# Kernel optimization log

Measured on AMD Instinct MI355X. Metric: run time of the kernel, lower is better.

Reference implementation:

```python
import jax, jax.numpy as jnp
import numpy as np

B, T, D, H = 16384, 48, 32, 64  # batch, num_lags, input_dim(num_features), hidden_size


def setup_inputs() -> dict:
    key = jax.random.key(0)
    ks = jax.random.split(key, 8)
    s = 1.0 / np.sqrt(H)  # torch-style uniform bound magnitude, approximated via scaled normal
    return {
        "x": jax.random.normal(ks[0], (B, T, D), dtype=jnp.float32),
        "h0": jax.random.normal(ks[1], (B, H), dtype=jnp.float32) * 0.01,
        "c0": jax.random.normal(ks[2], (B, H), dtype=jnp.float32) * 0.01,
        "W_att": jax.random.normal(ks[3], (1, 2 * H + T), dtype=jnp.float32) * 0.05,
        "b_att": jnp.zeros((1,), dtype=jnp.float32),
        "W_ih": jax.random.normal(ks[4], (4 * H, D), dtype=jnp.float32) * s,
        "W_hh": jax.random.normal(ks[5], (4 * H, H), dtype=jnp.float32) * s,
        "b_ih": jnp.zeros((4 * H,), dtype=jnp.float32),
        "b_hh": jnp.zeros((4 * H,), dtype=jnp.float32),
    }


def reference(x, h0, c0, W_att, b_att, W_ih, W_hh, b_ih, b_hh):
    # x: [B, T, D];  input-attention DA-RNN encoder with single-layer LSTM.
    Bn, Tn, Dn = x.shape
    Hn = h0.shape[-1]
    xT = jnp.transpose(x, (0, 2, 1))  # [B, D, T] full per-feature series, constant over t
    w_att = W_att[0]                   # [2H+T]

    def step(carry, xt):
        ht, ct = carry  # [B, H]
        hrep = jnp.broadcast_to(ht[:, None, :], (Bn, Dn, Hn))
        crep = jnp.broadcast_to(ct[:, None, :], (Bn, Dn, Hn))
        feat = jnp.concatenate([hrep, crep, xT], axis=2)  # [B, D, 2H+T]
        et = jnp.einsum('bdf,f->bd', feat, w_att) + b_att[0]  # [B, D]
        at = jax.nn.softmax(et, axis=1)                        # softmax over features
        wi = at * xt                                           # [B, D]
        gates = wi @ W_ih.T + b_ih + ht @ W_hh.T + b_hh        # [B, 4H]
        i_g, f_g, g_g, o_g = jnp.split(gates, 4, axis=1)
        i_g = jax.nn.sigmoid(i_g)
        f_g = jax.nn.sigmoid(f_g)
        g_g = jnp.tanh(g_g)
        o_g = jax.nn.sigmoid(o_g)
        ct2 = f_g * ct + i_g * g_g
        ht2 = o_g * jnp.tanh(ct2)
        return (ht2, ct2), (at, ht2)

    xs = jnp.transpose(x, (1, 0, 2))  # [T, B, D]
    _, (ats, hts) = jax.lax.scan(step, (h0, c0), xs)
    attention = jnp.transpose(ats, (1, 0, 2))       # [B, T, D]
    input_encoded = jnp.transpose(hts, (1, 0, 2))   # [B, T, H]
    return attention, input_encoded
```

## Files before the change

kernel.cpp:

```cpp
#include <hip/hip_runtime.h>

#define TT 48
#define DD 32
#define HH 64
#define BB 16384
#define LOG2E 1.4426950408889634f

typedef __bf16 bf16x8 __attribute__((ext_vector_type(8)));
typedef float f32x4 __attribute__((ext_vector_type(4)));

#define MFMA(a, b, c) __builtin_amdgcn_mfma_f32_16x16x32_bf16(a, b, c, 0, 0, 0)
#define BC(v) __builtin_bit_cast(bf16x8, v)

static __device__ __forceinline__ float exp2_f(float v) {
#if __has_builtin(__builtin_amdgcn_exp2f)
  return __builtin_amdgcn_exp2f(v);
#else
  return exp2f(v);
#endif
}
static __device__ __forceinline__ unsigned short bfu(float f) {
  __bf16 b = (__bf16)f;
  return __builtin_bit_cast(unsigned short, b);
}
static __device__ __forceinline__ float sigm2(float y) {
  return __builtin_amdgcn_rcpf(1.f + exp2_f(-y));
}
static __device__ __forceinline__ float tanh2(float y) {
  return fmaf(-2.f, __builtin_amdgcn_rcpf(1.f + exp2_f(y)), 1.f);
}


__global__ void prep_kernel(const float* __restrict__ W_ih, const float* __restrict__ W_hh,
                            const float* __restrict__ b_ih, const float* __restrict__ b_hh,
                            unsigned short* __restrict__ WhhL, unsigned short* __restrict__ WihL,
                            float* __restrict__ bsumL) {
  const int tid = threadIdx.x;
  const int l = tid & 63, qt = tid >> 6;
  const int rowl = l & 15, kq = (l >> 4) * 8;
  for (int mm = 0; mm < 4; ++mm) {
    const int m = qt * 4 + mm;
    const int g = m >> 2, hq = m & 3;
    const float s = (g == 2) ? 2.f * LOG2E : LOG2E;
    const int hidx = (hq >> 1) * 32 + (rowl >> 2) * 8 + (hq & 1) * 4 + (rowl & 3);
    const int orig = g * 64 + hidx;
    for (int c = 0; c < 2; ++c)
      for (int j = 0; j < 8; ++j)
        WhhL[(m * 2 + c) * 512 + l * 8 + j] = bfu(W_hh[orig * 64 + c * 32 + kq + j] * s);
    for (int j = 0; j < 8; ++j)
      WihL[m * 512 + l * 8 + j] = bfu(W_ih[orig * 32 + kq + j] * s);
    if ((l >> 4) == 0) bsumL[m * 16 + rowl] = (b_ih[orig] + b_hh[orig]) * s;
  }
}

__global__ __launch_bounds__(256) void attn_kernel(const float* __restrict__ x,
                                                   const float* __restrict__ W_att,
                                                   float* __restrict__ out0) {
  int tid = threadIdx.x;
  int b = blockIdx.x * 32 + (tid >> 3);
  int dq = (tid & 7) * 4;
  const float* xb = x + (size_t)b * (TT * DD);
  float px = 0.f, py = 0.f, pz = 0.f, pw = 0.f;
#pragma unroll 4
  for (int t = 0; t < TT; ++t) {
    float w = W_att[2 * HH + t];
    float4 xv = *(const float4*)(xb + t * DD + dq);
    px = fmaf(xv.x, w, px);
    py = fmaf(xv.y, w, py);
    pz = fmaf(xv.z, w, pz);
    pw = fmaf(xv.w, w, pw);
  }
  float m = fmaxf(fmaxf(px, py), fmaxf(pz, pw));
#pragma unroll
  for (int s = 1; s < 8; s <<= 1) m = fmaxf(m, __shfl_xor(m, s));
  float ex = __expf(px - m), ey = __expf(py - m), ez = __expf(pz - m), ew = __expf(pw - m);
  float sum = ex + ey + ez + ew;
#pragma unroll
  for (int s = 1; s < 8; s <<= 1) sum += __shfl_xor(sum, s);
  float inv = __builtin_amdgcn_rcpf(sum);
  float4 a;
  a.x = ex * inv; a.y = ey * inv; a.z = ez * inv; a.w = ew * inv;
  float* o = out0 + (size_t)b * (TT * DD) + dq;
#pragma unroll 4
  for (int t = 0; t < TT; ++t) *(float4*)(o + t * DD) = a;
}

__global__ __launch_bounds__(256, 1) void lstm_kernel(
    const float* __restrict__ x, const float* __restrict__ h0, const float* __restrict__ c0,
    const float* __restrict__ a_src, const unsigned short* __restrict__ WhhL,
    const unsigned short* __restrict__ WihL, const float* __restrict__ bsumL,
    float* __restrict__ out1) {
  const int tid = threadIdx.x;
  const int l = tid & 63;
  const int wid = tid >> 6;
  const int b = l & 15;
  const int qp = l >> 4;
  const int brow = blockIdx.x * 64 + wid * 16 + b;

  f32x4 whhHi[16][2], wihR[16], biasR[16];
#pragma unroll
  for (int m = 0; m < 16; ++m) {
#pragma unroll
    for (int c = 0; c < 2; ++c)
      whhHi[m][c] = *(const f32x4*)(WhhL + ((m * 2 + c) << 9) + l * 8);
    wihR[m] = *(const f32x4*)(WihL + (m << 9) + l * 8);
    biasR[m] = *(const f32x4*)(bsumL + m * 16 + qp * 4);
  }
#pragma unroll
  for (int m = 0; m < 16; ++m) {
#pragma unroll
    for (int c = 0; c < 2; ++c) asm volatile("" : "+v"(whhHi[m][c]));
    asm volatile("" : "+a"(wihR[m]));
    asm volatile("" : "+a"(biasR[m]));
  }

  float av[8];
  {
    const float* ap = a_src + (size_t)brow * (TT * DD) + qp * 8;
    float4 a0 = *(const float4*)ap, a1 = *(const float4*)(ap + 4);
    av[0] = a0.x; av[1] = a0.y; av[2] = a0.z; av[3] = a0.w;
    av[4] = a1.x; av[5] = a1.y; av[6] = a1.z; av[7] = a1.w;
  }

  f32x4 creg[4];
#pragma unroll
  for (int hq = 0; hq < 4; ++hq)
    creg[hq] = *(const f32x4*)(c0 + (size_t)brow * HH + (hq >> 1) * 32 + qp * 8 + (hq & 1) * 4);

  bf16x8 bh[2];
#pragma unroll
  for (int c = 0; c < 2; ++c) {
    const float* hp = h0 + (size_t)brow * HH + c * 32 + qp * 8;
    float4 v0 = *(const float4*)hp, v1 = *(const float4*)(hp + 4);
    float vv[8] = {v0.x, v0.y, v0.z, v0.w, v1.x, v1.y, v1.z, v1.w};
#pragma unroll
    for (int j = 0; j < 8; ++j) bh[c][j] = (__bf16)vv[j];
  }

  const float* xp = x + (size_t)brow * (TT * DD) + qp * 8;
  float* op = out1 + (size_t)brow * (TT * HH);
  float xv[8];
  {
    float4 x0 = *(const float4*)xp, x1 = *(const float4*)(xp + 4);
    xv[0] = x0.x; xv[1] = x0.y; xv[2] = x0.z; xv[3] = x0.w;
    xv[4] = x1.x; xv[5] = x1.y; xv[6] = x1.z; xv[7] = x1.w;
  }

#pragma unroll 1
  for (int t = 0; t < TT; ++t) {
    bf16x8 bxw;
#pragma unroll
    for (int j = 0; j < 8; ++j) bxw[j] = (__bf16)(xv[j] * av[j]);
    const int tn = (t + 1 < TT) ? (t + 1) : (TT - 1);
    float xn[8];
    {
      const float* xnp = xp + (size_t)tn * DD;
      float4 x0 = *(const float4*)xnp, x1 = *(const float4*)(xnp + 4);
      xn[0] = x0.x; xn[1] = x0.y; xn[2] = x0.z; xn[3] = x0.w;
      xn[4] = x1.x; xn[5] = x1.y; xn[6] = x1.z; xn[7] = x1.w;
    }

    bf16x8 nbh[2];
#pragma unroll
    for (int hq = 0; hq < 4; ++hq) {
      f32x4 acc[4];
#pragma unroll
      for (int g = 0; g < 4; ++g) {
        const int m = g * 4 + hq;
        f32x4 A = MFMA(BC(whhHi[m][0]), bh[0], biasR[m]);
        A = MFMA(BC(whhHi[m][1]), bh[1], A);
        A = MFMA(BC(wihR[m]), bxw, A);
        acc[g] = A;
      }
      float hr[4];
#pragma unroll
      for (int r = 0; r < 4; ++r) {
        float ig = sigm2(acc[0][r]);
        float fg = sigm2(acc[1][r]);
        float gt = tanh2(acc[2][r]);
        float og = sigm2(acc[3][r]);
        float cn = fg * creg[hq][r] + ig * gt;
        creg[hq][r] = cn;
        hr[r] = og * tanh2(2.f * LOG2E * cn);
      }
      float4 hv;
      hv.x = hr[0]; hv.y = hr[1]; hv.z = hr[2]; hv.w = hr[3];
      *(float4*)(op + (size_t)t * HH + (hq >> 1) * 32 + qp * 8 + (hq & 1) * 4) = hv;
#pragma unroll
      for (int r = 0; r < 4; ++r) nbh[hq >> 1][(hq & 1) * 4 + r] = (__bf16)hr[r];
    }
    bh[0] = nbh[0];
    bh[1] = nbh[1];
#pragma unroll
    for (int j = 0; j < 8; ++j) xv[j] = xn[j];
  }
}

extern "C" void kernel_launch(void* const* d_in, const int* in_sizes, int n_in,
                              void* d_out, int out_size, void* d_ws, size_t ws_size,
                              hipStream_t stream) {
  const float* x = (const float*)d_in[0];
  const float* h0 = (const float*)d_in[1];
  const float* c0 = (const float*)d_in[2];
  const float* W_att = (const float*)d_in[3];
  const float* W_ih = (const float*)d_in[5];
  const float* W_hh = (const float*)d_in[6];
  const float* b_ih = (const float*)d_in[7];
  const float* b_hh = (const float*)d_in[8];

  float* out0 = (float*)d_out;
  float* out1 = out0 + (size_t)BB * TT * DD;

  char* ws = (char*)d_ws;
  unsigned short* WhhL = (unsigned short*)ws;
  unsigned short* WihL = (unsigned short*)(ws + 32768);
  float* bsumL = (float*)(ws + 49152);

  prep_kernel<<<1, 256, 0, stream>>>(W_ih, W_hh, b_ih, b_hh, WhhL, WihL, bsumL);
  attn_kernel<<<BB / 32, 256, 0, stream>>>(x, W_att, out0);
  lstm_kernel<<<BB / 64, 256, 0, stream>>>(x, h0, c0, out0, WhhL, WihL, bsumL, out1);
}
```

Baseline: 146.1 us.

## Fuse attention softmax into LSTM kernel and write attention output inside loop

Removes the separate attention kernel and computes the time-invariant attention softmax inside the LSTM kernel from x, using cross-lane shuffles over the four lane groups that cover the 32 features. Attention rows are stored per timestep inside the recurrent loop instead of in a separate pass. This drops one kernel launch and the write-then-reread of attention through global memory. In exchange, each LSTM block must first stream its x rows once before the recurrence, and the loop carries extra stores.

```diff
diff --git a/kernel.cpp b/kernel.cpp
--- a/kernel.cpp
+++ b/kernel.cpp
@@ -53,43 +53,11 @@
   }
 }
 
-__global__ __launch_bounds__(256) void attn_kernel(const float* __restrict__ x,
-                                                   const float* __restrict__ W_att,
-                                                   float* __restrict__ out0) {
-  int tid = threadIdx.x;
-  int b = blockIdx.x * 32 + (tid >> 3);
-  int dq = (tid & 7) * 4;
-  const float* xb = x + (size_t)b * (TT * DD);
-  float px = 0.f, py = 0.f, pz = 0.f, pw = 0.f;
-#pragma unroll 4
-  for (int t = 0; t < TT; ++t) {
-    float w = W_att[2 * HH + t];
-    float4 xv = *(const float4*)(xb + t * DD + dq);
-    px = fmaf(xv.x, w, px);
-    py = fmaf(xv.y, w, py);
-    pz = fmaf(xv.z, w, pz);
-    pw = fmaf(xv.w, w, pw);
-  }
-  float m = fmaxf(fmaxf(px, py), fmaxf(pz, pw));
-#pragma unroll
-  for (int s = 1; s < 8; s <<= 1) m = fmaxf(m, __shfl_xor(m, s));
-  float ex = __expf(px - m), ey = __expf(py - m), ez = __expf(pz - m), ew = __expf(pw - m);
-  float sum = ex + ey + ez + ew;
-#pragma unroll
-  for (int s = 1; s < 8; s <<= 1) sum += __shfl_xor(sum, s);
-  float inv = __builtin_amdgcn_rcpf(sum);
-  float4 a;
-  a.x = ex * inv; a.y = ey * inv; a.z = ez * inv; a.w = ew * inv;
-  float* o = out0 + (size_t)b * (TT * DD) + dq;
-#pragma unroll 4
-  for (int t = 0; t < TT; ++t) *(float4*)(o + t * DD) = a;
-}
-
 __global__ __launch_bounds__(256, 1) void lstm_kernel(
     const float* __restrict__ x, const float* __restrict__ h0, const float* __restrict__ c0,
-    const float* __restrict__ a_src, const unsigned short* __restrict__ WhhL,
+    const float* __restrict__ W_att, const unsigned short* __restrict__ WhhL,
     const unsigned short* __restrict__ WihL, const float* __restrict__ bsumL,
-    float* __restrict__ out1) {
+    float* __restrict__ out0, float* __restrict__ out1) {
   const int tid = threadIdx.x;
   const int l = tid & 63;
   const int wid = tid >> 6;
@@ -114,13 +82,43 @@
     asm volatile("" : "+a"(biasR[m]));
   }
 
+  const float* xp = x + (size_t)brow * (TT * DD) + qp * 8;
+
+  float p[8];
+#pragma unroll
+  for (int j = 0; j < 8; ++j) p[j] = 0.f;
+#pragma unroll 4
+  for (int t = 0; t < TT; ++t) {
+    const float w = W_att[2 * HH + t];
+    float4 x0 = *(const float4*)(xp + t * DD);
+    float4 x1 = *(const float4*)(xp + t * DD + 4);
+    p[0] = fmaf(x0.x, w, p[0]); p[1] = fmaf(x0.y, w, p[1]);
+    p[2] = fmaf(x0.z, w, p[2]); p[3] = fmaf(x0.w, w, p[3]);
+    p[4] = fmaf(x1.x, w, p[4]); p[5] = fmaf(x1.y, w, p[5]);
+    p[6] = fmaf(x1.z, w, p[6]); p[7] = fmaf(x1.w, w, p[7]);
+  }
   float av[8];
   {
-    const float* ap = a_src + (size_t)brow * (TT * DD) + qp * 8;
-    float4 a0 = *(const float4*)ap, a1 = *(const float4*)(ap + 4);
-    av[0] = a0.x; av[1] = a0.y; av[2] = a0.z; av[3] = a0.w;
-    av[4] = a1.x; av[5] = a1.y; av[6] = a1.z; av[7] = a1.w;
-  }
+    float mx = fmaxf(fmaxf(fmaxf(p[0], p[1]), fmaxf(p[2], p[3])),
+                     fmaxf(fmaxf(p[4], p[5]), fmaxf(p[6], p[7])));
+    mx = fmaxf(mx, __shfl_xor(mx, 16));
+    mx = fmaxf(mx, __shfl_xor(mx, 32));
+    float s = 0.f;
+#pragma unroll
+    for (int j = 0; j < 8; ++j) {
+      av[j] = exp2_f((p[j] - mx) * LOG2E);
+      s += av[j];
+    }
+    s += __shfl_xor(s, 16);
+    s += __shfl_xor(s, 32);
+    float inv = __builtin_amdgcn_rcpf(s);
+#pragma unroll
+    for (int j = 0; j < 8; ++j) av[j] *= inv;
+  }
+  float4 av0, av1;
+  av0.x = av[0]; av0.y = av[1]; av0.z = av[2]; av0.w = av[3];
+  av1.x = av[4]; av1.y = av[5]; av1.z = av[6]; av1.w = av[7];
+  float* o0 = out0 + (size_t)brow * (TT * DD) + qp * 8;
 
   f32x4 creg[4];
 #pragma unroll
@@ -137,7 +135,6 @@
     for (int j = 0; j < 8; ++j) bh[c][j] = (__bf16)vv[j];
   }
 
-  const float* xp = x + (size_t)brow * (TT * DD) + qp * 8;
   float* op = out1 + (size_t)brow * (TT * HH);
   float xv[8];
   {
@@ -148,6 +145,8 @@
 
 #pragma unroll 1
   for (int t = 0; t < TT; ++t) {
+    *(float4*)(o0 + t * DD) = av0;
+    *(float4*)(o0 + t * DD + 4) = av1;
     bf16x8 bxw;
 #pragma unroll
     for (int j = 0; j < 8; ++j) bxw[j] = (__bf16)(xv[j] * av[j]);
@@ -217,6 +216,5 @@
   float* bsumL = (float*)(ws + 49152);
 
   prep_kernel<<<1, 256, 0, stream>>>(W_ih, W_hh, b_ih, b_hh, WhhL, WihL, bsumL);
-  attn_kernel<<<BB / 32, 256, 0, stream>>>(x, W_att, out0);
-  lstm_kernel<<<BB / 64, 256, 0, stream>>>(x, h0, c0, out0, WhhL, WihL, bsumL, out1);
-}
+  lstm_kernel<<<BB / 64, 256, 0, stream>>>(x, h0, c0, W_att, WhhL, WihL, bsumL, out0, out1);
+}
```

After: 121.0 us. 1.21x faster.
